# Kernel tuning notes

Measured on AMD Instinct MI355X. Metric: run time of the kernel, lower is better.

Reference implementation:

```python
import jax, jax.numpy as jnp
import numpy as np

H = 25   # num heads
D = 128  # head dim
EPS = 1e-6

def rmsnorm(x, w):
    # RMSNorm over last dim (hidden=3200), computed in fp32
    var = jnp.mean(jnp.square(x.astype(jnp.float32)), axis=-1, keepdims=True)
    return (x.astype(jnp.float32) * jax.lax.rsqrt(var + EPS)).astype(x.dtype) * w


def setup_inputs() -> dict:
    key = jax.random.key(0)
    ks = jax.random.split(key, 4)
    B, N, C = 8, 1025, 3200
    x = jax.random.normal(ks[0], (B, N, C), dtype=jnp.float32)
    w_qkv = jax.random.normal(ks[1], (3 * C, C), dtype=jnp.float32) * (C ** -0.5)
    q_norm_w = jnp.ones((C,), dtype=jnp.float32)
    k_norm_w = jnp.ones((C,), dtype=jnp.float32)
    w_proj = jax.random.normal(ks[2], (C, C), dtype=jnp.float32) * (C ** -0.5)
    b_proj = jnp.zeros((C,), dtype=jnp.float32)
    return {"x": x, "w_qkv": w_qkv, "q_norm_w": q_norm_w,
            "k_norm_w": k_norm_w, "w_proj": w_proj, "b_proj": b_proj}


def reference(x, w_qkv, q_norm_w, k_norm_w, w_proj, b_proj):
    B, N, C = x.shape
    # fused QKV projection: [B,N,3C]
    qkv = jnp.einsum('bnc,oc->bno', x, w_qkv)
    q, k, v = qkv[..., :C], qkv[..., C:2 * C], qkv[..., 2 * C:]
    # per-tensor RMSNorm over the full hidden dim (flattened across heads)
    q = rmsnorm(q, q_norm_w)
    k = rmsnorm(k, k_norm_w)
    # split heads: [B,N,H,D]
    q = q.reshape(B, N, H, D)
    k = k.reshape(B, N, H, D)
    v = v.reshape(B, N, H, D)
    scale = 1.0 / np.sqrt(D)
    scores = jnp.einsum('bqhd,bkhd->bhqk', q, k) * scale
    attn = jax.nn.softmax(scores, axis=-1)
    out = jnp.einsum('bhqk,bkhd->bqhd', attn, v).reshape(B, N, C)
    return jnp.einsum('bnc,oc->bno', out, w_proj) + b_proj
```

## Files before the change

kernel.cpp:

```cpp
#include <hip/hip_runtime.h>
#include <hip/hip_bf16.h>

#define B_     8
#define N_     1025
#define C_     3200
#define H_     25
#define D_     128
#define NQKV   (3 * C_)
#define NQKVP  9728
#define M_REAL (B_ * N_)
#define M_PAD  8448
#define KVB    64
#define KPAD   1088

typedef __bf16 bf16x8 __attribute__((ext_vector_type(8)));
typedef short  short8 __attribute__((ext_vector_type(8)));
typedef float  f32x4  __attribute__((ext_vector_type(4)));
typedef unsigned int u32x4 __attribute__((ext_vector_type(4)));

__device__ __forceinline__ unsigned short f2bf(float f) {
    unsigned u = __builtin_bit_cast(unsigned, f);
    u += 0x7FFFu + ((u >> 16) & 1u);
    return (unsigned short)(u >> 16);
}
__device__ __forceinline__ float bf2f(unsigned short u) {
    unsigned v = ((unsigned)u) << 16;
    return __builtin_bit_cast(float, v);
}
__device__ __forceinline__ unsigned cvtpk_bf16(float lo, float hi) {
    unsigned r;
    asm("v_cvt_pk_bf16_f32 %0, %1, %2" : "=v"(r) : "v"(lo), "v"(hi));
    return r;
}
__device__ __forceinline__ void gload_lds16(const unsigned short* g, void* lds) {
    __builtin_amdgcn_global_load_lds(
        (const __attribute__((address_space(1))) void*)g,
        (__attribute__((address_space(3))) void*)lds, 16, 0, 0);
}

__global__ __launch_bounds__(256) void convert_pad(const float* __restrict__ src,
                                                   unsigned short* __restrict__ dst,
                                                   long n_src, long n_tot) {
    long e = ((long)blockIdx.x * 256 + threadIdx.x) * 4;
    if (e >= n_tot) return;
    ushort4 o;
    if (e < n_src) {
        float4 v = *reinterpret_cast<const float4*>(src + e);
        o.x = f2bf(v.x); o.y = f2bf(v.y); o.z = f2bf(v.z); o.w = f2bf(v.w);
    } else {
        o.x = o.y = o.z = o.w = 0;
    }
    *reinterpret_cast<ushort4*>(dst + e) = o;
}

__global__ __launch_bounds__(256) void rmsnorm_qk(unsigned short* __restrict__ qkv,
                                                  const float* __restrict__ qw,
                                                  const float* __restrict__ kw) {
    const int row = blockIdx.x;
    const int seg = blockIdx.y;
    unsigned short* p = qkv + (long)row * NQKVP + seg * C_;
    const float* w = seg ? kw : qw;
    const int t = threadIdx.x;
    const bool has2 = t < (400 - 256);

    short8 v0 = reinterpret_cast<const short8*>(p)[t];
    short8 v1;
    if (has2) v1 = reinterpret_cast<const short8*>(p)[t + 256];

    float s = 0.f;
#pragma unroll
    for (int j = 0; j < 8; ++j) { float f = bf2f((unsigned short)v0[j]); s += f * f; }
    if (has2) {
#pragma unroll
        for (int j = 0; j < 8; ++j) { float f = bf2f((unsigned short)v1[j]); s += f * f; }
    }
#pragma unroll
    for (int m = 32; m; m >>= 1) s += __shfl_xor(s, m);
    __shared__ float red[4];
    if ((t & 63) == 0) red[t >> 6] = s;
    __syncthreads();
    float tot = red[0] + red[1] + red[2] + red[3];
    float scale = rsqrtf(tot * (1.f / C_) + 1e-6f);
    if (seg == 0) scale *= 0.08838834764831845f;

#pragma unroll
    for (int j = 0; j < 8; ++j) {
        float f = bf2f((unsigned short)v0[j]) * scale * w[t * 8 + j];
        v0[j] = (short)f2bf(f);
    }
    reinterpret_cast<short8*>(p)[t] = v0;
    if (has2) {
#pragma unroll
        for (int j = 0; j < 8; ++j) {
            float f = bf2f((unsigned short)v1[j]) * scale * w[(t + 256) * 8 + j];
            v1[j] = (short)f2bf(f);
        }
        reinterpret_cast<short8*>(p)[t + 256] = v1;
    }
}

#define BKT 32
__global__ __launch_bounds__(512) void gemm_pipe(const unsigned short* __restrict__ A,
                                                 const unsigned short* __restrict__ Bm,
                                                 unsigned short* __restrict__ Cb,
                                                 int K, int MT, int GN, int nwg, int ldc) {
    __shared__ unsigned short sA[4][256 * BKT];
    __shared__ unsigned short sB[4][256 * BKT];

    int bid = blockIdx.x;
    int qq = nwg >> 3, rr = nwg & 7;
    int xcd = bid & 7, pos = bid >> 3;
    int v = (xcd < rr ? xcd * (qq + 1) : rr * (qq + 1) + (xcd - rr) * qq) + pos;
    int per = MT * GN;
    int strip = v / per, rem = v - strip * per;
    int nt = strip * GN + rem / MT, mt = rem % MT;
    const int m0 = mt * 256, n0 = nt * 256;

    const int t = threadIdx.x, w = t >> 6, l = t & 63;
    const int lq = l & 15, lh = l >> 4;
    const int wr = w >> 2, wc = w & 3;

    const unsigned short* Ab = A + (long)m0 * K;
    const unsigned short* Bb = Bm + (long)n0 * K;
    const int nk = K / BKT;

    const int c0 = t, c1 = t + 512;
    const int r0 = c0 >> 2, s0 = (c0 & 3) ^ (r0 & 3);
    const int r1 = c1 >> 2, s1 = (c1 & 3) ^ (r1 & 3);

    f32x4 acc[8][4] = {};

    auto stage = [&](int tile) {
        int k0 = tile * BKT;
        unsigned short* dA = sA[tile & 3];
        unsigned short* dB = sB[tile & 3];
        gload_lds16(Ab + (long)r0 * K + k0 + s0 * 8, (char*)dA + c0 * 16);
        gload_lds16(Ab + (long)r1 * K + k0 + s1 * 8, (char*)dA + c1 * 16);
        gload_lds16(Bb + (long)r0 * K + k0 + s0 * 8, (char*)dB + c0 * 16);
        gload_lds16(Bb + (long)r1 * K + k0 + s1 * 8, (char*)dB + c1 * 16);
    };

    stage(0); stage(1); stage(2);

    for (int tt = 0; tt < nk; ++tt) {
        if (tt + 2 < nk)      asm volatile("s_waitcnt vmcnt(8) lgkmcnt(0)" ::: "memory");
        else if (tt + 1 < nk) asm volatile("s_waitcnt vmcnt(4) lgkmcnt(0)" ::: "memory");
        else                  asm volatile("s_waitcnt vmcnt(0) lgkmcnt(0)" ::: "memory");
        __builtin_amdgcn_s_barrier();

        const unsigned short* bufA = sA[tt & 3];
        const unsigned short* bufB = sB[tt & 3];
        bf16x8 av[8], bv[4];
#pragma unroll
        for (int i = 0; i < 8; ++i) {
            int row = wr * 128 + i * 16 + lq;
            av[i] = *reinterpret_cast<const bf16x8*>(bufA + row * BKT + ((lh ^ (row & 3)) << 3));
        }
#pragma unroll
        for (int j = 0; j < 4; ++j) {
            int row = wc * 64 + j * 16 + lq;
            bv[j] = *reinterpret_cast<const bf16x8*>(bufB + row * BKT + ((lh ^ (row & 3)) << 3));
        }
        if (tt + 3 < nk) stage(tt + 3);

        __builtin_amdgcn_s_setprio(1);
#pragma unroll
        for (int i = 0; i < 8; ++i)
#pragma unroll
            for (int j = 0; j < 4; ++j)
                acc[i][j] = __builtin_amdgcn_mfma_f32_16x16x32_bf16(av[i], bv[j], acc[i][j], 0, 0, 0);
        __builtin_amdgcn_s_setprio(0);
    }

#pragma unroll
    for (int i = 0; i < 8; ++i) {
#pragma unroll
        for (int r2 = 0; r2 < 4; ++r2) {
            long grow = m0 + wr * 128 + i * 16 + lh * 4 + r2;
#pragma unroll
            for (int j = 0; j < 4; ++j) {
                int gcol = n0 + wc * 64 + j * 16 + lq;
                Cb[grow * ldc + gcol] = f2bf(acc[i][j][r2]);
            }
        }
    }
}

template <int BF16OUT>
__global__ __launch_bounds__(256) void gemm_bt(const unsigned short* __restrict__ A,
                                               const unsigned short* __restrict__ Bm,
                                               unsigned short* __restrict__ Cb,
                                               float* __restrict__ Cf,
                                               const float* __restrict__ bias,
                                               int M, int N, int K, int MStore) {
    const int t = threadIdx.x;
    const int w = t >> 6, l = t & 63;
    const int lq = l & 15, lh = l >> 4;
    const int m0 = blockIdx.y * 128, n0 = blockIdx.x * 128;
    const int wr = w >> 1, wc = w & 1;

    __shared__ unsigned short sA[128 * 32];
    __shared__ unsigned short sB[128 * 32];

    const f32x4 fz = {0.f, 0.f, 0.f, 0.f};
    f32x4 acc[4][4];
#pragma unroll
    for (int i = 0; i < 4; ++i)
#pragma unroll
        for (int j = 0; j < 4; ++j) acc[i][j] = fz;

    const unsigned short* Abase = A + (long)m0 * K;
    const unsigned short* Bbase = Bm + (long)n0 * K;

    for (int k0 = 0; k0 < K; k0 += 32) {
        __syncthreads();
#pragma unroll
        for (int i = 0; i < 2; ++i) {
            int c = i * 256 + t;
            int row = c >> 2, slot = c & 3;
            gload_lds16(Abase + (long)row * K + k0 + slot * 8, (char*)sA + c * 16);
            gload_lds16(Bbase + (long)row * K + k0 + slot * 8, (char*)sB + c * 16);
        }
        __syncthreads();

        bf16x8 av[4], bv[4];
#pragma unroll
        for (int i = 0; i < 4; ++i) {
            int row = wr * 64 + i * 16 + lq;
            av[i] = *reinterpret_cast<const bf16x8*>(sA + row * 32 + lh * 8);
        }
#pragma unroll
        for (int j = 0; j < 4; ++j) {
            int row = wc * 64 + j * 16 + lq;
            bv[j] = *reinterpret_cast<const bf16x8*>(sB + row * 32 + lh * 8);
        }
#pragma unroll
        for (int i = 0; i < 4; ++i)
#pragma unroll
            for (int j = 0; j < 4; ++j)
                acc[i][j] = __builtin_amdgcn_mfma_f32_16x16x32_bf16(av[i], bv[j], acc[i][j], 0, 0, 0);
    }

#pragma unroll
    for (int i = 0; i < 4; ++i) {
#pragma unroll
        for (int r = 0; r < 4; ++r) {
            int grow = m0 + wr * 64 + i * 16 + lh * 4 + r;
            if (grow >= MStore) continue;
#pragma unroll
            for (int j = 0; j < 4; ++j) {
                int gcol = n0 + wc * 64 + j * 16 + lq;
                float v = acc[i][j][r];
                if (BF16OUT)
                    Cb[(long)grow * N + gcol] = f2bf(v);
                else
                    Cf[(long)grow * N + gcol] = v + bias[gcol];
            }
        }
    }
}

__global__ __launch_bounds__(256) void v_transpose(const unsigned short* __restrict__ qkv,
                                                   unsigned short* __restrict__ vtb) {
    const int kt = blockIdx.x, h = blockIdx.y, b = blockIdx.z;
    const int t = threadIdx.x;
    __shared__ unsigned short tile[64][136];

    {
        int r = t >> 2, dq = (t & 3) * 32;
        int key = kt * 64 + r;
        int keyc = key < N_ ? key : N_ - 1;
        const unsigned short* src = qkv + ((long)(b * N_) + keyc) * NQKVP + 2 * C_ + h * D_ + dq;
        short8 a0 = *reinterpret_cast<const short8*>(src);
        short8 a1 = *reinterpret_cast<const short8*>(src + 8);
        short8 a2 = *reinterpret_cast<const short8*>(src + 16);
        short8 a3 = *reinterpret_cast<const short8*>(src + 24);
        if (key >= N_) { a0 = 0; a1 = 0; a2 = 0; a3 = 0; }
        *reinterpret_cast<short8*>(&tile[r][dq])      = a0;
        *reinterpret_cast<short8*>(&tile[r][dq + 8])  = a1;
        *reinterpret_cast<short8*>(&tile[r][dq + 16]) = a2;
        *reinterpret_cast<short8*>(&tile[r][dq + 24]) = a3;
    }
    __syncthreads();
    {
        int d = t >> 1, k0 = (t & 1) * 32;
        unsigned short* dst = vtb + ((long)(b * H_ + h) * D_ + d) * KPAD + kt * 64 + k0;
#pragma unroll
        for (int jj = 0; jj < 4; ++jj) {
            short8 g;
#pragma unroll
            for (int e = 0; e < 8; ++e) g[e] = (short)tile[k0 + jj * 8 + e][d];
            *reinterpret_cast<short8*>(dst + jj * 8) = g;
        }
    }
}

__global__ __launch_bounds__(256, 2) void attn_fwd(const unsigned short* __restrict__ qkv,
                                                   const unsigned short* __restrict__ vtb,
                                                   unsigned short* __restrict__ outb) {
    const int qt = blockIdx.x, h = blockIdx.y, b = blockIdx.z;
    const int t = threadIdx.x, w = t >> 6, l = t & 63;
    const int lq = l & 15, lh = l >> 4;

    __shared__ unsigned short sK[2][KVB * D_];
    __shared__ unsigned short sV[2][D_ * KVB];

    const int qbase = qt * 128 + w * 32;
    bf16x8 qf[2][4];
#pragma unroll
    for (int qg = 0; qg < 2; ++qg) {
        int qrow = qbase + qg * 16 + lq; if (qrow > N_ - 1) qrow = N_ - 1;
        const unsigned short* qp = qkv + (long)(b * N_ + qrow) * NQKVP + h * D_;
#pragma unroll
        for (int ds = 0; ds < 4; ++ds)
            qf[qg][ds] = *reinterpret_cast<const bf16x8*>(qp + ds * 32 + lh * 8);
    }

    const unsigned short* kp[4];
    const unsigned short* vp[4];
#pragma unroll
    for (int i = 0; i < 4; ++i) {
        int slot = i * 256 + t;
        { int r = slot >> 4, sd = (slot & 15) ^ (r & 7);
          kp[i] = qkv + ((long)(b * N_) + r) * NQKVP + C_ + h * D_ + sd * 8; }
        { int d = slot >> 3, sk = (slot & 7) ^ (d & 7);
          vp[i] = vtb + ((long)(b * H_ + h) * D_ + d) * KPAD + sk * 8; }
    }
    const long kvstep = 64L * NQKVP;

    auto stageK = [&](int tile, int buf) {
        char* dst = (char*)sK[buf];
        if (tile < 16) {
            long off = (long)tile * kvstep;
#pragma unroll
            for (int i = 0; i < 4; ++i) gload_lds16(kp[i] + off, dst + (i * 256 + t) * 16);
        } else {
#pragma unroll
            for (int i = 0; i < 4; ++i) {
                int slot = i * 256 + t;
                int r = slot >> 4, sd = (slot & 15) ^ (r & 7);
                const unsigned short* p = qkv + ((long)(b * N_) + (N_ - 1)) * NQKVP + C_ + h * D_ + sd * 8;
                gload_lds16(p, dst + slot * 16);
            }
        }
    };
    auto stageV = [&](int tile, int buf) {
        char* dst = (char*)sV[buf];
        long off = (long)tile * 64;
#pragma unroll
        for (int i = 0; i < 4; ++i) gload_lds16(vp[i] + off, dst + (i * 256 + t) * 16);
    };

    f32x4 o[2][8] = {};
    float m[2] = {-1e30f, -1e30f}, lsum[2] = {0.f, 0.f};

    stageK(0, 0); stageV(0, 0);

    for (int tt = 0; tt < 17; ++tt) {
        const int cur = tt & 1;
        if (tt < 16) { stageK(tt + 1, cur ^ 1); stageV(tt + 1, cur ^ 1); }
        if (tt < 16) asm volatile("s_waitcnt vmcnt(8)" ::: "memory");
        else         asm volatile("s_waitcnt vmcnt(0)" ::: "memory");
        __builtin_amdgcn_s_barrier();

        const unsigned short* bK = sK[cur];
        const unsigned short* bV = sV[cur];

        f32x4 s[2][4] = {};
#pragma unroll
        for (int c = 0; c < 4; ++c) {
            bf16x8 kf[4];
#pragma unroll
            for (int ds = 0; ds < 4; ++ds)
                kf[ds] = *reinterpret_cast<const bf16x8*>(
                    bK + (c * 16 + lq) * D_ + (((ds << 2) + lh) ^ (lq & 7)) * 8);
            __builtin_amdgcn_s_setprio(1);
#pragma unroll
            for (int qg = 0; qg < 2; ++qg)
#pragma unroll
                for (int ds = 0; ds < 4; ++ds)
                    s[qg][c] = __builtin_amdgcn_mfma_f32_16x16x32_bf16(kf[ds], qf[qg][ds], s[qg][c], 0, 0, 0);
            __builtin_amdgcn_s_setprio(0);
        }
        if (tt == 16) {
#pragma unroll
            for (int c = 0; c < 4; ++c)
#pragma unroll
                for (int r = 0; r < 4; ++r)
                    if (c * 16 + 4 * lh + r != 0) { s[0][c][r] = -1e30f; s[1][c][r] = -1e30f; }
        }

        bf16x8 pa[2][2];
#pragma unroll
        for (int qg = 0; qg < 2; ++qg) {
            float mx = s[qg][0][0];
#pragma unroll
            for (int c = 0; c < 4; ++c)
#pragma unroll
                for (int r = 0; r < 4; ++r) mx = fmaxf(mx, s[qg][c][r]);
            mx = fmaxf(mx, __shfl_xor(mx, 16));
            mx = fmaxf(mx, __shfl_xor(mx, 32));
            if (__any(mx - m[qg] > 8.0f)) {
                float mnew = fmaxf(m[qg], mx);
                float corr = __expf(m[qg] - mnew);
                lsum[qg] *= corr;
#pragma unroll
                for (int r = 0; r < 4; ++r) {
                    float co = __shfl(corr, lh * 4 + r);
#pragma unroll
                    for (int nf = 0; nf < 8; ++nf) o[qg][nf][r] *= co;
                }
                m[qg] = mnew;
            }
            float p[4][4]; float rs = 0.f;
#pragma unroll
            for (int c = 0; c < 4; ++c)
#pragma unroll
                for (int r = 0; r < 4; ++r) {
                    p[c][r] = __expf(s[qg][c][r] - m[qg]);
                    rs += p[c][r];
                }
            rs += __shfl_xor(rs, 16);
            rs += __shfl_xor(rs, 32);
            lsum[qg] += rs;
#pragma unroll
            for (int h2 = 0; h2 < 2; ++h2) {
                unsigned A0 = cvtpk_bf16(p[2 * h2][0], p[2 * h2][1]);
                unsigned A1 = cvtpk_bf16(p[2 * h2][2], p[2 * h2][3]);
                unsigned B0 = cvtpk_bf16(p[2 * h2 + 1][0], p[2 * h2 + 1][1]);
                unsigned B1 = cvtpk_bf16(p[2 * h2 + 1][2], p[2 * h2 + 1][3]);
                const bool lo2 = lh < 2, odd = lh & 1;
                unsigned x16_0 = __shfl_xor(lo2 ? A0 : B0, 16);
                unsigned x16_1 = __shfl_xor(lo2 ? A1 : B1, 16);
                unsigned x32_0 = __shfl_xor(lo2 ? B0 : A0, 32);
                unsigned x32_1 = __shfl_xor(lo2 ? B1 : A1, 32);
                unsigned x48_0 = __shfl_xor(odd ? B0 : A0, 48);
                unsigned x48_1 = __shfl_xor(odd ? B1 : A1, 48);
                unsigned w0 = lh == 0 ? A0 : lh == 1 ? x48_0 : lh == 2 ? x32_0 : x16_0;
                unsigned w1 = lh == 0 ? A1 : lh == 1 ? x48_1 : lh == 2 ? x32_1 : x16_1;
                unsigned w2 = lh == 0 ? x16_0 : lh == 1 ? x32_0 : lh == 2 ? x48_0 : B0;
                unsigned w3 = lh == 0 ? x16_1 : lh == 1 ? x32_1 : lh == 2 ? x48_1 : B1;
                u32x4 wv = {w0, w1, w2, w3};
                pa[qg][h2] = __builtin_bit_cast(bf16x8, wv);
            }
        }

#pragma unroll
        for (int h2 = 0; h2 < 2; ++h2) {
            bf16x8 vf[8];
#pragma unroll
            for (int nf = 0; nf < 8; ++nf)
                vf[nf] = *reinterpret_cast<const bf16x8*>(
                    bV + (nf * 16 + lq) * KVB + (((h2 << 2) + lh) ^ (lq & 7)) * 8);
            __builtin_amdgcn_s_setprio(1);
#pragma unroll
            for (int qg = 0; qg < 2; ++qg)
#pragma unroll
                for (int nf = 0; nf < 8; ++nf)
                    o[qg][nf] = __builtin_amdgcn_mfma_f32_16x16x32_bf16(pa[qg][h2], vf[nf], o[qg][nf], 0, 0, 0);
            __builtin_amdgcn_s_setprio(0);
        }
        __builtin_amdgcn_s_barrier();
    }

#pragma unroll
    for (int qg = 0; qg < 2; ++qg) {
        float linv = 1.f / lsum[qg];
#pragma unroll
        for (int r = 0; r < 4; ++r) {
            float li = __shfl(linv, lh * 4 + r);
            int row = qbase + qg * 16 + 4 * lh + r;
            if (row < N_) {
                unsigned short* dst = outb + (long)(b * N_ + row) * C_ + h * D_ + lq;
#pragma unroll
                for (int nf = 0; nf < 8; ++nf)
                    dst[nf * 16] = f2bf(o[qg][nf][r] * li);
            }
        }
    }
}

extern "C" void kernel_launch(void* const* d_in, const int* in_sizes, int n_in,
                              void* d_out, int out_size, void* d_ws, size_t ws_size,
                              hipStream_t stream) {
    (void)in_sizes; (void)n_in; (void)out_size; (void)ws_size;
    const float* x   = (const float*)d_in[0];
    const float* wq  = (const float*)d_in[1];
    const float* qnw = (const float*)d_in[2];
    const float* knw = (const float*)d_in[3];
    const float* wp  = (const float*)d_in[4];
    const float* bp  = (const float*)d_in[5];
    float* out = (float*)d_out;

    unsigned short* xb    = (unsigned short*)d_ws;
    unsigned short* wqb   = xb   + (size_t)M_PAD * C_;
    unsigned short* wpb   = wqb  + (size_t)NQKVP * C_;
    unsigned short* qkvb  = wpb  + (size_t)C_ * C_;
    unsigned short* attnb = qkvb + (size_t)M_PAD * NQKVP;
    unsigned short* vtb   = wqb;

    auto cvt = [&](const float* s, unsigned short* d, long nsrc, long ntot) {
        int blocks = (int)((ntot / 4 + 255) / 256);
        convert_pad<<<blocks, 256, 0, stream>>>(s, d, nsrc, ntot);
    };
    cvt(x,  xb,  (long)M_REAL * C_, (long)M_PAD * C_);
    cvt(wq, wqb, (long)NQKV * C_,   (long)NQKVP * C_);
    cvt(wp, wpb, (long)C_ * C_,     (long)C_ * C_);
    cvt(x, attnb + (size_t)M_REAL * C_, 0, (long)(M_PAD - M_REAL) * C_);

    {
        const int MT = M_PAD / 256;
        const int NT = NQKVP / 256;
        const int nwg = MT * NT;
        gemm_pipe<<<nwg, 512, 0, stream>>>(xb, wqb, qkvb, C_, MT, 4, nwg, NQKVP);
    }

    rmsnorm_qk<<<dim3(M_REAL, 2), 256, 0, stream>>>(qkvb, qnw, knw);

    v_transpose<<<dim3(17, H_, B_), 256, 0, stream>>>(qkvb, vtb);

    attn_fwd<<<dim3(9, H_, B_), 256, 0, stream>>>(qkvb, vtb, attnb);

    gemm_bt<0><<<dim3(C_ / 128, M_PAD / 128), 256, 0, stream>>>(
        attnb, wpb, nullptr, out, bp, M_PAD, C_, C_, M_REAL);
}
```

Baseline: 1.158 ms.

## Run output projection through pipelined 256x256 GEMM with fp32 bias epilogue

Replaces the simple single-buffered 128x128 gemm_bt used for the output projection with the 4-stage pipelined 256x256 gemm_pipe kernel, templated for an fp32+bias epilogue with row and column bounds. Pads w_proj to 3328 rows so N divides by 256, changes the block-to-XCD mapping so each XCD handles one N column strip, and alters the LDS swizzle to use (row>>1)&3. This targets the poorly pipelined projection GEMM and L2 locality, at the cost of wasted padded columns and a tile count that may leave some CUs idle.

After: 1.056 ms (median of 3 runs). 1.1x faster.

```diff
diff --git a/kernel.cpp b/kernel.cpp
--- a/kernel.cpp
+++ b/kernel.cpp
@@ -12,6 +12,7 @@
 #define M_PAD  8448
 #define KVB    64
 #define KPAD   1088
+#define CPADW  3328
 
 typedef __bf16 bf16x8 __attribute__((ext_vector_type(8)));
 typedef short  short8 __attribute__((ext_vector_type(8)));
@@ -100,20 +101,31 @@
 }
 
 #define BKT 32
+template <int FP32OUT>
 __global__ __launch_bounds__(512) void gemm_pipe(const unsigned short* __restrict__ A,
                                                  const unsigned short* __restrict__ Bm,
                                                  unsigned short* __restrict__ Cb,
-                                                 int K, int MT, int GN, int nwg, int ldc) {
+                                                 float* __restrict__ Cf,
+                                                 const float* __restrict__ bias,
+                                                 int K, int MT, int NT, int ldc,
+                                                 int MStore, int NStore) {
     __shared__ unsigned short sA[4][256 * BKT];
     __shared__ unsigned short sB[4][256 * BKT];
 
     int bid = blockIdx.x;
-    int qq = nwg >> 3, rr = nwg & 7;
     int xcd = bid & 7, pos = bid >> 3;
-    int v = (xcd < rr ? xcd * (qq + 1) : rr * (qq + 1) + (xcd - rr) * qq) + pos;
-    int per = MT * GN;
-    int strip = v / per, rem = v - strip * per;
-    int nt = strip * GN + rem / MT, mt = rem % MT;
+    int nstrips = NT >> 3;
+    int fullpos = nstrips * MT;
+    int mt, nt;
+    if (pos < fullpos) {
+        int strip = pos / MT;
+        mt = pos - strip * MT;
+        nt = strip * 8 + xcd;
+    } else {
+        int lin = bid - fullpos * 8;
+        nt = nstrips * 8 + lin / MT;
+        mt = lin - (lin / MT) * MT;
+    }
     const int m0 = mt * 256, n0 = nt * 256;
 
     const int t = threadIdx.x, w = t >> 6, l = t & 63;
@@ -125,8 +137,8 @@
     const int nk = K / BKT;
 
     const int c0 = t, c1 = t + 512;
-    const int r0 = c0 >> 2, s0 = (c0 & 3) ^ (r0 & 3);
-    const int r1 = c1 >> 2, s1 = (c1 & 3) ^ (r1 & 3);
+    const int r0 = c0 >> 2, s0 = (c0 & 3) ^ ((r0 >> 1) & 3);
+    const int r1 = c1 >> 2, s1 = (c1 & 3) ^ ((r1 >> 1) & 3);
 
     f32x4 acc[8][4] = {};
 
@@ -154,12 +166,12 @@
 #pragma unroll
         for (int i = 0; i < 8; ++i) {
             int row = wr * 128 + i * 16 + lq;
-            av[i] = *reinterpret_cast<const bf16x8*>(bufA + row * BKT + ((lh ^ (row & 3)) << 3));
+            av[i] = *reinterpret_cast<const bf16x8*>(bufA + row * BKT + ((lh ^ ((row >> 1) & 3)) << 3));
         }
 #pragma unroll
         for (int j = 0; j < 4; ++j) {
             int row = wc * 64 + j * 16 + lq;
-            bv[j] = *reinterpret_cast<const bf16x8*>(bufB + row * BKT + ((lh ^ (row & 3)) << 3));
+            bv[j] = *reinterpret_cast<const bf16x8*>(bufB + row * BKT + ((lh ^ ((row >> 1) & 3)) << 3));
         }
         if (tt + 3 < nk) stage(tt + 3);
 
@@ -177,84 +189,16 @@
 #pragma unroll
         for (int r2 = 0; r2 < 4; ++r2) {
             long grow = m0 + wr * 128 + i * 16 + lh * 4 + r2;
+            if (FP32OUT && grow >= MStore) continue;
 #pragma unroll
             for (int j = 0; j < 4; ++j) {
                 int gcol = n0 + wc * 64 + j * 16 + lq;
-                Cb[grow * ldc + gcol] = f2bf(acc[i][j][r2]);
-            }
-        }
-    }
-}
-
-template <int BF16OUT>
-__global__ __launch_bounds__(256) void gemm_bt(const unsigned short* __restrict__ A,
-                                               const unsigned short* __restrict__ Bm,
-                                               unsigned short* __restrict__ Cb,
-                                               float* __restrict__ Cf,
-                                               const float* __restrict__ bias,
-                                               int M, int N, int K, int MStore) {
-    const int t = threadIdx.x;
-    const int w = t >> 6, l = t & 63;
-    const int lq = l & 15, lh = l >> 4;
-    const int m0 = blockIdx.y * 128, n0 = blockIdx.x * 128;
-    const int wr = w >> 1, wc = w & 1;
-
-    __shared__ unsigned short sA[128 * 32];
-    __shared__ unsigned short sB[128 * 32];
-
-    const f32x4 fz = {0.f, 0.f, 0.f, 0.f};
-    f32x4 acc[4][4];
-#pragma unroll
-    for (int i = 0; i < 4; ++i)
-#pragma unroll
-        for (int j = 0; j < 4; ++j) acc[i][j] = fz;
-
-    const unsigned short* Abase = A + (long)m0 * K;
-    const unsigned short* Bbase = Bm + (long)n0 * K;
-
-    for (int k0 = 0; k0 < K; k0 += 32) {
-        __syncthreads();
-#pragma unroll
-        for (int i = 0; i < 2; ++i) {
-            int c = i * 256 + t;
-            int row = c >> 2, slot = c & 3;
-            gload_lds16(Abase + (long)row * K + k0 + slot * 8, (char*)sA + c * 16);
-            gload_lds16(Bbase + (long)row * K + k0 + slot * 8, (char*)sB + c * 16);
-        }
-        __syncthreads();
-
-        bf16x8 av[4], bv[4];
-#pragma unroll
-        for (int i = 0; i < 4; ++i) {
-            int row = wr * 64 + i * 16 + lq;
-            av[i] = *reinterpret_cast<const bf16x8*>(sA + row * 32 + lh * 8);
-        }
-#pragma unroll
-        for (int j = 0; j < 4; ++j) {
-            int row = wc * 64 + j * 16 + lq;
-            bv[j] = *reinterpret_cast<const bf16x8*>(sB + row * 32 + lh * 8);
-        }
-#pragma unroll
-        for (int i = 0; i < 4; ++i)
-#pragma unroll
-            for (int j = 0; j < 4; ++j)
-                acc[i][j] = __builtin_amdgcn_mfma_f32_16x16x32_bf16(av[i], bv[j], acc[i][j], 0, 0, 0);
-    }
-
-#pragma unroll
-    for (int i = 0; i < 4; ++i) {
-#pragma unroll
-        for (int r = 0; r < 4; ++r) {
-            int grow = m0 + wr * 64 + i * 16 + lh * 4 + r;
-            if (grow >= MStore) continue;
-#pragma unroll
-            for (int j = 0; j < 4; ++j) {
-                int gcol = n0 + wc * 64 + j * 16 + lq;
-                float v = acc[i][j][r];
-                if (BF16OUT)
-                    Cb[(long)grow * N + gcol] = f2bf(v);
-                else
-                    Cf[(long)grow * N + gcol] = v + bias[gcol];
+                if (FP32OUT) {
+                    if (gcol < NStore)
+                        Cf[grow * ldc + gcol] = acc[i][j][r2] + bias[gcol];
+                } else {
+                    Cb[grow * ldc + gcol] = f2bf(acc[i][j][r2]);
+                }
             }
         }
     }
@@ -495,7 +439,7 @@
     unsigned short* xb    = (unsigned short*)d_ws;
     unsigned short* wqb   = xb   + (size_t)M_PAD * C_;
     unsigned short* wpb   = wqb  + (size_t)NQKVP * C_;
-    unsigned short* qkvb  = wpb  + (size_t)C_ * C_;
+    unsigned short* qkvb  = wpb  + (size_t)CPADW * C_;
     unsigned short* attnb = qkvb + (size_t)M_PAD * NQKVP;
     unsigned short* vtb   = wqb;
 
@@ -505,15 +449,11 @@
     };
     cvt(x,  xb,  (long)M_REAL * C_, (long)M_PAD * C_);
     cvt(wq, wqb, (long)NQKV * C_,   (long)NQKVP * C_);
-    cvt(wp, wpb, (long)C_ * C_,     (long)C_ * C_);
+    cvt(wp, wpb, (long)C_ * C_,     (long)CPADW * C_);
     cvt(x, attnb + (size_t)M_REAL * C_, 0, (long)(M_PAD - M_REAL) * C_);
 
-    {
-        const int MT = M_PAD / 256;
-        const int NT = NQKVP / 256;
-        const int nwg = MT * NT;
-        gemm_pipe<<<nwg, 512, 0, stream>>>(xb, wqb, qkvb, C_, MT, 4, nwg, NQKVP);
-    }
+    gemm_pipe<0><<<(M_PAD / 256) * (NQKVP / 256), 512, 0, stream>>>(
+        xb, wqb, qkvb, nullptr, nullptr, C_, M_PAD / 256, NQKVP / 256, NQKVP, M_PAD, NQKVP);
 
     rmsnorm_qk<<<dim3(M_REAL, 2), 256, 0, stream>>>(qkvb, qnw, knw);
 
@@ -521,6 +461,6 @@
 
     attn_fwd<<<dim3(9, H_, B_), 256, 0, stream>>>(qkvb, vtb, attnb);
 
-    gemm_bt<0><<<dim3(C_ / 128, M_PAD / 128), 256, 0, stream>>>(
-        attnb, wpb, nullptr, out, bp, M_PAD, C_, C_, M_REAL);
-}
+    gemm_pipe<1><<<(M_PAD / 256) * (CPADW / 256), 512, 0, stream>>>(
+        attnb, wpb, nullptr, out, bp, C_, M_PAD / 256, CPADW / 256, C_, M_REAL, C_);
+}
```
